# Optimization experiments

Measured on AMD Instinct MI355X. Metric: run time of the kernel, lower is better.

## Reference

```python
import jax, jax.numpy as jnp
import numpy as np

B = 131072
FEATURES = 64
NUM_BINS = 10
HIDDEN = 512
TAIL_BOUND = 1.0
MIN_BIN_WIDTH = 1e-3
MIN_BIN_HEIGHT = 1e-3
MIN_DERIVATIVE = 1e-3

# alternating mask [1,0,1,0,...]: mask>0 -> transform features, mask<=0 -> identity features
TRANSFORM_IDX = np.arange(0, FEATURES, 2)
IDENTITY_IDX = np.arange(1, FEATURES, 2)
D_ID = len(IDENTITY_IDX)   # 32
D_TR = len(TRANSFORM_IDX)  # 32
PARAM_PER_FEAT = 3 * NUM_BINS - 1  # tails='linear' -> 29
PARAM_DIM = D_TR * PARAM_PER_FEAT  # 928


def setup_inputs() -> dict:
    key = jax.random.key(0)
    k = jax.random.split(key, 3)
    x = jax.random.normal(k[0], (B, FEATURES), jnp.float32)
    W1 = jax.random.normal(k[1], (D_ID, HIDDEN), jnp.float32) / np.sqrt(D_ID)
    b1 = jnp.zeros((HIDDEN,), jnp.float32)
    W2 = jax.random.normal(k[2], (HIDDEN, PARAM_DIM), jnp.float32) / np.sqrt(HIDDEN)
    b2 = jnp.zeros((PARAM_DIM,), jnp.float32)
    return {"x": x, "W1": W1, "b1": b1, "W2": W2, "b2": b2}


def _rqs(x, uw, uh, ud):
    """Unconstrained rational-quadratic spline with linear tails, forward direction.
    x: [B, D]; uw, uh: [B, D, NUM_BINS]; ud: [B, D, NUM_BINS-1].
    Returns (outputs [B,D], logabsdet [B,D])."""
    inside = (x >= -TAIL_BOUND) & (x <= TAIL_BOUND)
    xc = jnp.clip(x, -TAIL_BOUND, TAIL_BOUND)
    # pad derivatives so boundary derivatives equal 1 (softplus(const)+md == 1)
    const = np.log(np.exp(1.0 - MIN_DERIVATIVE) - 1.0)
    ud = jnp.pad(ud, [(0, 0), (0, 0), (1, 1)], constant_values=const)
    nb = NUM_BINS

    widths = jax.nn.softmax(uw, axis=-1)
    widths = MIN_BIN_WIDTH + (1 - MIN_BIN_WIDTH * nb) * widths
    cumw = jnp.pad(jnp.cumsum(widths, axis=-1), [(0, 0), (0, 0), (1, 0)])
    cumw = 2 * TAIL_BOUND * cumw - TAIL_BOUND
    cumw = cumw.at[..., 0].set(-TAIL_BOUND).at[..., -1].set(TAIL_BOUND)
    widths = cumw[..., 1:] - cumw[..., :-1]

    derivs = MIN_DERIVATIVE + jax.nn.softplus(ud)  # [B, D, nb+1]

    heights = jax.nn.softmax(uh, axis=-1)
    heights = MIN_BIN_HEIGHT + (1 - MIN_BIN_HEIGHT * nb) * heights
    cumh = jnp.pad(jnp.cumsum(heights, axis=-1), [(0, 0), (0, 0), (1, 0)])
    cumh = 2 * TAIL_BOUND * cumh - TAIL_BOUND
    cumh = cumh.at[..., 0].set(-TAIL_BOUND).at[..., -1].set(TAIL_BOUND)
    heights = cumh[..., 1:] - cumh[..., :-1]

    # bin search (nflows-style searchsorted with eps on last edge)
    locs = cumw.at[..., -1].add(1e-6)
    idx = jnp.sum((xc[..., None] >= locs).astype(jnp.int32), axis=-1) - 1
    idx = jnp.clip(idx, 0, nb - 1)[..., None]

    g = lambda t: jnp.take_along_axis(t, idx, axis=-1)[..., 0]
    in_cw = g(cumw)
    in_w = g(widths)
    in_ch = g(cumh)
    in_h = g(heights)
    in_delta = g(heights / widths)
    d_k = g(derivs)
    d_k1 = jnp.take_along_axis(derivs, idx + 1, axis=-1)[..., 0]

    theta = (xc - in_cw) / in_w
    t1m = theta * (1 - theta)
    numer = in_h * (in_delta * theta ** 2 + d_k * t1m)
    denom = in_delta + (d_k + d_k1 - 2 * in_delta) * t1m
    y = in_ch + numer / denom
    dnum = in_delta ** 2 * (d_k1 * theta ** 2 + 2 * in_delta * t1m + d_k * (1 - theta) ** 2)
    lad = jnp.log(dnum) - 2 * jnp.log(denom)
    # linear tails: identity outside [-B, B], logabsdet 0
    return jnp.where(inside, y, x), jnp.where(inside, lad, 0.0)


def reference(x, W1, b1, W2, b2):
    ident = x[:, IDENTITY_IDX]   # [B, D_ID]
    trans = x[:, TRANSFORM_IDX]  # [B, D_TR]
    # transform_net: 1-hidden-layer MLP
    h = jax.nn.relu(ident @ W1 + b1)
    params = (h @ W2 + b2).reshape(x.shape[0], D_TR, PARAM_PER_FEAT)
    scale = 1.0 / np.sqrt(HIDDEN)  # hidden_features scaling branch
    uw = params[..., :NUM_BINS] * scale
    uh = params[..., NUM_BINS:2 * NUM_BINS] * scale
    ud = params[..., 2 * NUM_BINS:]
    y_tr, lad = _rqs(trans, uw, uh, ud)
    logabsdet = jnp.sum(lad, axis=1)  # sum_except_batch
    out = jnp.zeros_like(x).at[:, IDENTITY_IDX].set(ident).at[:, TRANSFORM_IDX].set(y_tr)
    ot_cost = jnp.sum((x - out) ** 2, axis=-1)
    return out, logabsdet, ot_cost
```

## Files before the change

### kernel.cpp

```cpp
#include <hip/hip_runtime.h>
#include <math.h>

#define NROWS 131072
#define BM 64
#define NBLK (NROWS / BM)
#define NB 10
#define PPF 29
#define NRAW 928
#define NPAD 1024
#define HID 512
#define THREADS 512

typedef _Float16 half8 __attribute__((ext_vector_type(8)));
typedef _Float16 half4v __attribute__((ext_vector_type(4)));
typedef float f32x4 __attribute__((ext_vector_type(4)));

#define W1T_OFF (NPAD * HID * 2)

#define LDS_B0 65536
#define LDS_B1 98304
#define LDS_TOTAL 131072
#define PSTR 937

__global__ __launch_bounds__(256) void prep_w2(const float* __restrict__ W2,
                                               _Float16* __restrict__ W2T) {
    __shared__ float tile[32][33];
    const int kt = blockIdx.x >> 5;
    const int nt = blockIdx.x & 31;
    const int t = threadIdx.x;
    const int j = t & 31;
    const int i0 = t >> 5;
    #pragma unroll
    for (int q = 0; q < 4; ++q) {
        int i = i0 + q * 8;
        int n = nt * 32 + j;
        float v = 0.f;
        if (n < NRAW) v = W2[(size_t)(kt * 32 + i) * NRAW + n];
        tile[i][j] = v;
    }
    __syncthreads();
    const int n_l = t >> 3;
    const int k_l = (t & 7) * 4;
    half4v o;
    o[0] = (_Float16)tile[k_l + 0][n_l];
    o[1] = (_Float16)tile[k_l + 1][n_l];
    o[2] = (_Float16)tile[k_l + 2][n_l];
    o[3] = (_Float16)tile[k_l + 3][n_l];
    *(half4v*)&W2T[(size_t)(nt * 32 + n_l) * HID + kt * 32 + k_l] = o;
}

__global__ __launch_bounds__(256) void prep_w1(const float* __restrict__ W1,
                                               _Float16* __restrict__ W1T) {
    int idx = blockIdx.x * 256 + threadIdx.x;
    int n = idx >> 5, k = idx & 31;
    W1T[n * 32 + k] = (_Float16)W1[k * HID + n];
}

__device__ __forceinline__ float softplusf(float v) {
    return fmaxf(v, 0.f) + log1pf(expf(-fabsf(v)));
}

__device__ __forceinline__ void rqs_one(const float* p, float xv, float& yo,
                                        float& lad_o, float& ot_o) {
    const float SCALE = 0.04419417382415922f;
    float uw[NB];
    #pragma unroll
    for (int j = 0; j < NB; ++j) uw[j] = p[j] * SCALE;
    float mw = uw[0];
    #pragma unroll
    for (int j = 1; j < NB; ++j) mw = fmaxf(mw, uw[j]);
    float sw = 0.f;
    #pragma unroll
    for (int j = 0; j < NB; ++j) { uw[j] = expf(uw[j] - mw); sw += uw[j]; }
    float invw = 1.f / sw;
    float cw[NB + 1];
    cw[0] = -1.f;
    float cum = 0.f;
    #pragma unroll
    for (int j = 0; j < NB; ++j) {
        cum += 0.001f + 0.99f * uw[j] * invw;
        cw[j + 1] = 2.f * cum - 1.f;
    }
    cw[NB] = 1.f;

    float uh[NB];
    #pragma unroll
    for (int j = 0; j < NB; ++j) uh[j] = p[NB + j] * SCALE;
    float mh = uh[0];
    #pragma unroll
    for (int j = 1; j < NB; ++j) mh = fmaxf(mh, uh[j]);
    float sh = 0.f;
    #pragma unroll
    for (int j = 0; j < NB; ++j) { uh[j] = expf(uh[j] - mh); sh += uh[j]; }
    float invh = 1.f / sh;
    float ch[NB + 1];
    ch[0] = -1.f;
    float cumh = 0.f;
    #pragma unroll
    for (int j = 0; j < NB; ++j) {
        cumh += 0.001f + 0.99f * uh[j] * invh;
        ch[j + 1] = 2.f * cumh - 1.f;
    }
    ch[NB] = 1.f;

    float dv[NB + 1];
    dv[0] = 1.0f;
    dv[NB] = 1.0f;
    #pragma unroll
    for (int j = 0; j < NB - 1; ++j) dv[j + 1] = 0.001f + softplusf(p[2 * NB + j]);

    float xc = fminf(fmaxf(xv, -1.f), 1.f);
    int idx = 0;
    #pragma unroll
    for (int j = 1; j <= NB - 1; ++j) idx += (xc >= cw[j]) ? 1 : 0;
    float in_cw = cw[0], cwn = cw[1];
    float in_ch = ch[0], chn = ch[1];
    float dk = dv[0], dk1 = dv[1];
    #pragma unroll
    for (int j = 1; j <= NB - 1; ++j) {
        bool cnd = (idx >= j);
        in_cw = cnd ? cw[j] : in_cw;
        cwn   = cnd ? cw[j + 1] : cwn;
        in_ch = cnd ? ch[j] : in_ch;
        chn   = cnd ? ch[j + 1] : chn;
        dk    = cnd ? dv[j] : dk;
        dk1   = cnd ? dv[j + 1] : dk1;
    }
    float in_w  = cwn - in_cw;
    float in_h  = chn - in_ch;
    float delta = in_h / in_w;
    float th    = (xc - in_cw) / in_w;
    float t1m   = th * (1.f - th);
    float th2   = th * th;
    float numer = in_h * (delta * th2 + dk * t1m);
    float denom = delta + (dk + dk1 - 2.f * delta) * t1m;
    float y     = in_ch + numer / denom;
    float omt   = 1.f - th;
    float dnum  = delta * delta * (dk1 * th2 + 2.f * delta * t1m + dk * omt * omt);
    float lad   = logf(dnum) - 2.f * logf(denom);

    bool inside = (xv >= -1.f) && (xv <= 1.f);
    yo = inside ? y : xv;
    lad_o = inside ? lad : 0.f;
    float dd = xv - yo;
    ot_o = dd * dd;
}

__global__ __launch_bounds__(THREADS, 2) void flow_main(
    const float* __restrict__ x,
    const float* __restrict__ b1,
    const float* __restrict__ b2,
    const _Float16* __restrict__ W2T,
    const _Float16* __restrict__ W1T,
    float* __restrict__ out,
    float* __restrict__ lad_out,
    float* __restrict__ ot_out)
{
    __shared__ __align__(16) char smem[LDS_TOTAL];
    __shared__ float sb2[NRAW];
    const int tid = threadIdx.x;
    const int w   = tid >> 6;
    const int l   = tid & 63;
    const int l15 = l & 15;
    const int g   = l >> 4;
    const int row0 = blockIdx.x * BM;

    {
        const float4* xv = (const float4*)(x + (size_t)row0 * 64);
        float4* ov = (float4*)(out + (size_t)row0 * 64);
        ov[tid] = xv[tid];
        ov[tid + 512] = xv[tid + 512];
    }
    sb2[tid] = b2[tid];
    if (tid < NRAW - 512) sb2[tid + 512] = b2[tid + 512];

    float4 st[4];
    #pragma unroll
    for (int q = 0; q < 4; ++q) {
        int s = tid + 512 * q;
        int nl = s >> 2, gg = s & 3;
        st[q] = *(const float4*)((const char*)W2T + (size_t)nl * (HID * 2) + gg * 16);
    }

    {
        const int mt1 = w >> 1;
        const int nbase = (w & 1) * 256;
        half8 a1;
        {
            const float4* xr = (const float4*)(x + (size_t)(row0 + mt1 * 16 + l15) * 64 + g * 16);
            float4 q0 = xr[0], q1 = xr[1], q2 = xr[2], q3 = xr[3];
            a1[0] = (_Float16)q0.y; a1[1] = (_Float16)q0.w;
            a1[2] = (_Float16)q1.y; a1[3] = (_Float16)q1.w;
            a1[4] = (_Float16)q2.y; a1[5] = (_Float16)q2.w;
            a1[6] = (_Float16)q3.y; a1[7] = (_Float16)q3.w;
        }
        #pragma unroll
        for (int j = 0; j < 16; ++j) {
            int n = nbase + j * 16 + l15;
            half8 bf = *(const half8*)((const char*)W1T + (size_t)n * 64 + g * 16);
            f32x4 c = {0.f, 0.f, 0.f, 0.f};
            c = __builtin_amdgcn_mfma_f32_16x16x32_f16(a1, bf, c, 0, 0, 0);
            float bias = b1[n];
            int srow_base = mt1 * 16 + g * 4;
            int sslot = n >> 3;
            #pragma unroll
            for (int r = 0; r < 4; ++r) {
                float hv = fmaxf(c[r] + bias, 0.f);
                int row = srow_base + r;
                int addr = row * 1024 + ((sslot ^ (row & 7)) << 4) + (n & 7) * 2;
                *(_Float16*)(smem + addr) = (_Float16)hv;
            }
        }
    }
    #pragma unroll
    for (int q = 0; q < 4; ++q) {
        int s = tid + 512 * q;
        int nl = s >> 2, gg = s & 3;
        int line = nl >> 1;
        int pos = (gg + 4 * (nl & 1)) ^ (line & 7);
        *(float4*)(smem + LDS_B0 + line * 128 + pos * 16) = st[q];
    }
    __syncthreads();

    f32x4 acc[4][8];
    #pragma unroll
    for (int mt = 0; mt < 4; ++mt)
        #pragma unroll
        for (int i = 0; i < 8; ++i) acc[mt][i] = (f32x4){0.f, 0.f, 0.f, 0.f};

    const int bn0 = w * 16 + l15;

    for (int ks = 0; ks < 16; ++ks) {
        #pragma unroll
        for (int q = 0; q < 4; ++q) {
            int s = tid + 512 * q;
            int nl = s >> 2, gg = s & 3;
            st[q] = *(const float4*)((const char*)W2T +
                     (size_t)(512 + nl) * (HID * 2) + ks * 64 + gg * 16);
        }
        half8 af[4];
        #pragma unroll
        for (int mt = 0; mt < 4; ++mt) {
            int row = mt * 16 + l15;
            int sslot = ks * 4 + g;
            af[mt] = *(const half8*)(smem + row * 1024 + ((sslot ^ (row & 7)) << 4));
        }
        #pragma unroll
        for (int i2 = 0; i2 < 4; ++i2) {
            int nloc = bn0 + i2 * 128;
            int line = nloc >> 1;
            int pos = (g + 4 * (nloc & 1)) ^ (line & 7);
            half8 bf = *(const half8*)(smem + LDS_B0 + line * 128 + pos * 16);
            acc[0][i2] = __builtin_amdgcn_mfma_f32_16x16x32_f16(af[0], bf, acc[0][i2], 0, 0, 0);
            acc[1][i2] = __builtin_amdgcn_mfma_f32_16x16x32_f16(af[1], bf, acc[1][i2], 0, 0, 0);
            acc[2][i2] = __builtin_amdgcn_mfma_f32_16x16x32_f16(af[2], bf, acc[2][i2], 0, 0, 0);
            acc[3][i2] = __builtin_amdgcn_mfma_f32_16x16x32_f16(af[3], bf, acc[3][i2], 0, 0, 0);
        }
        #pragma unroll
        for (int q = 0; q < 4; ++q) {
            int s = tid + 512 * q;
            int nl = s >> 2, gg = s & 3;
            int line = nl >> 1;
            int pos = (gg + 4 * (nl & 1)) ^ (line & 7);
            *(float4*)(smem + LDS_B1 + line * 128 + pos * 16) = st[q];
        }
        __syncthreads();

        if (ks < 15) {
            #pragma unroll
            for (int q = 0; q < 4; ++q) {
                int s = tid + 512 * q;
                int nl = s >> 2, gg = s & 3;
                st[q] = *(const float4*)((const char*)W2T +
                         (size_t)nl * (HID * 2) + (ks + 1) * 64 + gg * 16);
            }
        }
        #pragma unroll
        for (int i2 = 0; i2 < 4; ++i2) {
            int nloc = bn0 + i2 * 128;
            int line = nloc >> 1;
            int pos = (g + 4 * (nloc & 1)) ^ (line & 7);
            half8 bf = *(const half8*)(smem + LDS_B1 + line * 128 + pos * 16);
            acc[0][4 + i2] = __builtin_amdgcn_mfma_f32_16x16x32_f16(af[0], bf, acc[0][4 + i2], 0, 0, 0);
            acc[1][4 + i2] = __builtin_amdgcn_mfma_f32_16x16x32_f16(af[1], bf, acc[1][4 + i2], 0, 0, 0);
            acc[2][4 + i2] = __builtin_amdgcn_mfma_f32_16x16x32_f16(af[2], bf, acc[2][4 + i2], 0, 0, 0);
            acc[3][4 + i2] = __builtin_amdgcn_mfma_f32_16x16x32_f16(af[3], bf, acc[3][4 + i2], 0, 0, 0);
        }
        if (ks < 15) {
            #pragma unroll
            for (int q = 0; q < 4; ++q) {
                int s = tid + 512 * q;
                int nl = s >> 2, gg = s & 3;
                int line = nl >> 1;
                int pos = (gg + 4 * (nl & 1)) ^ (line & 7);
                *(float4*)(smem + LDS_B0 + line * 128 + pos * 16) = st[q];
            }
        }
        __syncthreads();
    }

    #pragma unroll
    for (int mh = 0; mh < 2; ++mh) {
        __syncthreads();
        #pragma unroll
        for (int mt2 = 0; mt2 < 2; ++mt2) {
            #pragma unroll
            for (int i = 0; i < 8; ++i) {
                int ntile = w + 8 * i;
                if (ntile < 58) {
                    int n = ntile * 16 + l15;
                    int prow = mt2 * 16 + g * 4;
                    #pragma unroll
                    for (int r = 0; r < 4; ++r) {
                        *(float*)(smem + ((prow + r) * PSTR + n) * 4) =
                            acc[mh * 2 + mt2][i][r];
                    }
                }
            }
        }
        __syncthreads();

        int row_l = tid >> 4;
        int grow = row0 + mh * 32 + row_l;
        float lads[2], ots[2];
        #pragma unroll
        for (int ff = 0; ff < 2; ++ff) {
            int f = (tid & 15) * 2 + ff;
            float p[PPF];
            #pragma unroll
            for (int j = 0; j < PPF; ++j)
                p[j] = *(const float*)(smem + (row_l * PSTR + f * PPF + j) * 4)
                       + sb2[f * PPF + j];
            float xv = x[(size_t)grow * 64 + 2 * f];
            float yo, lo, oo;
            rqs_one(p, xv, yo, lo, oo);
            out[(size_t)grow * 64 + 2 * f] = yo;
            lads[ff] = lo;
            ots[ff] = oo;
        }
        float ladp = lads[0] + lads[1];
        float otp  = ots[0] + ots[1];
        #pragma unroll
        for (int m = 1; m < 16; m <<= 1) {
            ladp += __shfl_xor(ladp, m);
            otp  += __shfl_xor(otp, m);
        }
        if ((tid & 15) == 0) {
            lad_out[grow] = ladp;
            ot_out[grow]  = otp;
        }
    }
}

extern "C" void kernel_launch(void* const* d_in, const int* in_sizes, int n_in,
                              void* d_out, int out_size, void* d_ws, size_t ws_size,
                              hipStream_t stream) {
    const float* x  = (const float*)d_in[0];
    const float* W1 = (const float*)d_in[1];
    const float* b1 = (const float*)d_in[2];
    const float* W2 = (const float*)d_in[3];
    const float* b2 = (const float*)d_in[4];
    float* out = (float*)d_out;
    float* lad = out + (size_t)NROWS * 64;
    float* otc = lad + NROWS;

    char* wsb = (char*)d_ws;
    _Float16* W2T = (_Float16*)wsb;
    _Float16* W1T = (_Float16*)(wsb + W1T_OFF);

    hipLaunchKernelGGL(prep_w2, dim3(512), dim3(256), 0, stream, W2, W2T);
    hipLaunchKernelGGL(prep_w1, dim3(64), dim3(256), 0, stream, W1, W1T);
    hipLaunchKernelGGL(flow_main, dim3(NBLK), dim3(THREADS), 0, stream,
                       x, b1, b2, W2T, W1T, out, lad, otc);
}
```

Measured before the change: 491.7 us.

## Hold A fragments in registers and stream W2 directly from global memory

The second GEMM no longer stages W2 tiles in LDS with double-buffering and barriers. Each wave keeps its 16-row slice of the hidden activations in registers across all K steps and reads W2 fragments straight from global memory (L2-resident) for half of the output columns. LDS shrinks to a padded hidden buffer that is reused for the parameter epilogue, which now runs in four 16-row passes with one row per 32 lanes. This removes LDS traffic and barriers from the main loop, but each wave now loads W2 from global/L2 instead of sharing it through LDS, raises register pressure with 32 accumulators plus 16 fragments, and splits columns unevenly between the two wave halves (16 vs 13 tile pairs).

```diff
diff --git a/kernel.cpp b/kernel.cpp
--- a/kernel.cpp
+++ b/kernel.cpp
@@ -17,10 +17,9 @@
 
 #define W1T_OFF (NPAD * HID * 2)
 
-#define LDS_B0 65536
-#define LDS_B1 98304
-#define LDS_TOTAL 131072
-#define PSTR 937
+#define HSTR 1040
+#define PSTR 936
+#define SMEM_BYTES (BM * HSTR)
 
 __global__ __launch_bounds__(256) void prep_w2(const float* __restrict__ W2,
                                                _Float16* __restrict__ W2T) {
@@ -146,6 +145,23 @@
     ot_o = dd * dd;
 }
 
+template<int NPAIR>
+__device__ __forceinline__ void gemm2_run(f32x4 (&acc)[32], const half8 (&afk)[16],
+                                          const char* w2b) {
+    #pragma unroll
+    for (int jp = 0; jp < NPAIR; ++jp) {
+        const char* p0 = w2b + (size_t)jp * 32768;
+        const char* p1 = p0 + 16384;
+        #pragma unroll
+        for (int ks = 0; ks < 16; ++ks) {
+            half8 bf0 = *(const half8*)(p0 + ks * 64);
+            half8 bf1 = *(const half8*)(p1 + ks * 64);
+            acc[2 * jp]     = __builtin_amdgcn_mfma_f32_16x16x32_f16(afk[ks], bf0, acc[2 * jp], 0, 0, 0);
+            acc[2 * jp + 1] = __builtin_amdgcn_mfma_f32_16x16x32_f16(afk[ks], bf1, acc[2 * jp + 1], 0, 0, 0);
+        }
+    }
+}
+
 __global__ __launch_bounds__(THREADS, 2) void flow_main(
     const float* __restrict__ x,
     const float* __restrict__ b1,
@@ -156,7 +172,7 @@
     float* __restrict__ lad_out,
     float* __restrict__ ot_out)
 {
-    __shared__ __align__(16) char smem[LDS_TOTAL];
+    __shared__ __align__(16) char smem[SMEM_BYTES];
     __shared__ float sb2[NRAW];
     const int tid = threadIdx.x;
     const int w   = tid >> 6;
@@ -164,6 +180,8 @@
     const int l15 = l & 15;
     const int g   = l >> 4;
     const int row0 = blockIdx.x * BM;
+    const int mt1 = w >> 1;
+    const int nh  = w & 1;
 
     {
         const float4* xv = (const float4*)(x + (size_t)row0 * 64);
@@ -174,17 +192,8 @@
     sb2[tid] = b2[tid];
     if (tid < NRAW - 512) sb2[tid + 512] = b2[tid + 512];
 
-    float4 st[4];
-    #pragma unroll
-    for (int q = 0; q < 4; ++q) {
-        int s = tid + 512 * q;
-        int nl = s >> 2, gg = s & 3;
-        st[q] = *(const float4*)((const char*)W2T + (size_t)nl * (HID * 2) + gg * 16);
-    }
-
     {
-        const int mt1 = w >> 1;
-        const int nbase = (w & 1) * 256;
+        const int nbase = nh * 256;
         half8 a1;
         {
             const float4* xr = (const float4*)(x + (size_t)(row0 + mt1 * 16 + l15) * 64 + g * 16);
@@ -201,151 +210,68 @@
             f32x4 c = {0.f, 0.f, 0.f, 0.f};
             c = __builtin_amdgcn_mfma_f32_16x16x32_f16(a1, bf, c, 0, 0, 0);
             float bias = b1[n];
-            int srow_base = mt1 * 16 + g * 4;
-            int sslot = n >> 3;
             #pragma unroll
             for (int r = 0; r < 4; ++r) {
                 float hv = fmaxf(c[r] + bias, 0.f);
-                int row = srow_base + r;
-                int addr = row * 1024 + ((sslot ^ (row & 7)) << 4) + (n & 7) * 2;
-                *(_Float16*)(smem + addr) = (_Float16)hv;
+                *(_Float16*)(smem + (mt1 * 16 + g * 4 + r) * HSTR + n * 2) = (_Float16)hv;
             }
         }
     }
+    __syncthreads();
+
+    half8 afk[16];
+    {
+        const char* abase = smem + (mt1 * 16 + l15) * HSTR + g * 16;
+        #pragma unroll
+        for (int ks = 0; ks < 16; ++ks)
+            afk[ks] = *(const half8*)(abase + ks * 64);
+    }
+
+    f32x4 acc[32];
+    #pragma unroll
+    for (int i = 0; i < 32; ++i) acc[i] = (f32x4){0.f, 0.f, 0.f, 0.f};
+
+    const char* w2b = (const char*)W2T + ((size_t)(nh * 512 + l15) * (HID * 2) + g * 16);
+    if (nh == 0) gemm2_run<16>(acc, afk, w2b);
+    else         gemm2_run<13>(acc, afk, w2b);
+
     #pragma unroll
     for (int q = 0; q < 4; ++q) {
-        int s = tid + 512 * q;
-        int nl = s >> 2, gg = s & 3;
-        int line = nl >> 1;
-        int pos = (gg + 4 * (nl & 1)) ^ (line & 7);
-        *(float4*)(smem + LDS_B0 + line * 128 + pos * 16) = st[q];
-    }
-    __syncthreads();
-
-    f32x4 acc[4][8];
-    #pragma unroll
-    for (int mt = 0; mt < 4; ++mt)
-        #pragma unroll
-        for (int i = 0; i < 8; ++i) acc[mt][i] = (f32x4){0.f, 0.f, 0.f, 0.f};
-
-    const int bn0 = w * 16 + l15;
-
-    for (int ks = 0; ks < 16; ++ks) {
-        #pragma unroll
-        for (int q = 0; q < 4; ++q) {
-            int s = tid + 512 * q;
-            int nl = s >> 2, gg = s & 3;
-            st[q] = *(const float4*)((const char*)W2T +
-                     (size_t)(512 + nl) * (HID * 2) + ks * 64 + gg * 16);
-        }
-        half8 af[4];
-        #pragma unroll
-        for (int mt = 0; mt < 4; ++mt) {
-            int row = mt * 16 + l15;
-            int sslot = ks * 4 + g;
-            af[mt] = *(const half8*)(smem + row * 1024 + ((sslot ^ (row & 7)) << 4));
-        }
-        #pragma unroll
-        for (int i2 = 0; i2 < 4; ++i2) {
-            int nloc = bn0 + i2 * 128;
-            int line = nloc >> 1;
-            int pos = (g + 4 * (nloc & 1)) ^ (line & 7);
-            half8 bf = *(const half8*)(smem + LDS_B0 + line * 128 + pos * 16);
-            acc[0][i2] = __builtin_amdgcn_mfma_f32_16x16x32_f16(af[0], bf, acc[0][i2], 0, 0, 0);
-            acc[1][i2] = __builtin_amdgcn_mfma_f32_16x16x32_f16(af[1], bf, acc[1][i2], 0, 0, 0);
-            acc[2][i2] = __builtin_amdgcn_mfma_f32_16x16x32_f16(af[2], bf, acc[2][i2], 0, 0, 0);
-            acc[3][i2] = __builtin_amdgcn_mfma_f32_16x16x32_f16(af[3], bf, acc[3][i2], 0, 0, 0);
-        }
-        #pragma unroll
-        for (int q = 0; q < 4; ++q) {
-            int s = tid + 512 * q;
-            int nl = s >> 2, gg = s & 3;
-            int line = nl >> 1;
-            int pos = (gg + 4 * (nl & 1)) ^ (line & 7);
-            *(float4*)(smem + LDS_B1 + line * 128 + pos * 16) = st[q];
-        }
         __syncthreads();
-
-        if (ks < 15) {
+        if (mt1 == q) {
             #pragma unroll
-            for (int q = 0; q < 4; ++q) {
-                int s = tid + 512 * q;
-                int nl = s >> 2, gg = s & 3;
-                st[q] = *(const float4*)((const char*)W2T +
-                         (size_t)nl * (HID * 2) + (ks + 1) * 64 + gg * 16);
-            }
-        }
-        #pragma unroll
-        for (int i2 = 0; i2 < 4; ++i2) {
-            int nloc = bn0 + i2 * 128;
-            int line = nloc >> 1;
-            int pos = (g + 4 * (nloc & 1)) ^ (line & 7);
-            half8 bf = *(const half8*)(smem + LDS_B1 + line * 128 + pos * 16);
-            acc[0][4 + i2] = __builtin_amdgcn_mfma_f32_16x16x32_f16(af[0], bf, acc[0][4 + i2], 0, 0, 0);
-            acc[1][4 + i2] = __builtin_amdgcn_mfma_f32_16x16x32_f16(af[1], bf, acc[1][4 + i2], 0, 0, 0);
-            acc[2][4 + i2] = __builtin_amdgcn_mfma_f32_16x16x32_f16(af[2], bf, acc[2][4 + i2], 0, 0, 0);
-            acc[3][4 + i2] = __builtin_amdgcn_mfma_f32_16x16x32_f16(af[3], bf, acc[3][4 + i2], 0, 0, 0);
-        }
-        if (ks < 15) {
-            #pragma unroll
-            for (int q = 0; q < 4; ++q) {
-                int s = tid + 512 * q;
-                int nl = s >> 2, gg = s & 3;
-                int line = nl >> 1;
-                int pos = (gg + 4 * (nl & 1)) ^ (line & 7);
-                *(float4*)(smem + LDS_B0 + line * 128 + pos * 16) = st[q];
-            }
-        }
-        __syncthreads();
-    }
-
-    #pragma unroll
-    for (int mh = 0; mh < 2; ++mh) {
-        __syncthreads();
-        #pragma unroll
-        for (int mt2 = 0; mt2 < 2; ++mt2) {
-            #pragma unroll
-            for (int i = 0; i < 8; ++i) {
-                int ntile = w + 8 * i;
-                if (ntile < 58) {
-                    int n = ntile * 16 + l15;
-                    int prow = mt2 * 16 + g * 4;
-                    #pragma unroll
-                    for (int r = 0; r < 4; ++r) {
-                        *(float*)(smem + ((prow + r) * PSTR + n) * 4) =
-                            acc[mh * 2 + mt2][i][r];
+            for (int j2 = 0; j2 < 32; ++j2) {
+                int n = nh * 512 + j2 * 16 + l15;
+                if (nh == 0 || j2 < 26) {
+                    if (n < NRAW) {
+                        #pragma unroll
+                        for (int r = 0; r < 4; ++r)
+                            *(float*)(smem + ((g * 4 + r) * PSTR + n) * 4) = acc[j2][r];
                     }
                 }
             }
         }
         __syncthreads();
 
-        int row_l = tid >> 4;
-        int grow = row0 + mh * 32 + row_l;
-        float lads[2], ots[2];
-        #pragma unroll
-        for (int ff = 0; ff < 2; ++ff) {
-            int f = (tid & 15) * 2 + ff;
-            float p[PPF];
-            #pragma unroll
-            for (int j = 0; j < PPF; ++j)
-                p[j] = *(const float*)(smem + (row_l * PSTR + f * PPF + j) * 4)
-                       + sb2[f * PPF + j];
-            float xv = x[(size_t)grow * 64 + 2 * f];
-            float yo, lo, oo;
-            rqs_one(p, xv, yo, lo, oo);
-            out[(size_t)grow * 64 + 2 * f] = yo;
-            lads[ff] = lo;
-            ots[ff] = oo;
-        }
-        float ladp = lads[0] + lads[1];
-        float otp  = ots[0] + ots[1];
-        #pragma unroll
-        for (int m = 1; m < 16; m <<= 1) {
+        int row_l = tid >> 5;
+        int f = tid & 31;
+        int grow = row0 + q * 16 + row_l;
+        float p[PPF];
+        #pragma unroll
+        for (int jj = 0; jj < PPF; ++jj)
+            p[jj] = *(const float*)(smem + (row_l * PSTR + f * PPF + jj) * 4)
+                    + sb2[f * PPF + jj];
+        float xv = x[(size_t)grow * 64 + 2 * f];
+        float yo, lo, oo;
+        rqs_one(p, xv, yo, lo, oo);
+        out[(size_t)grow * 64 + 2 * f] = yo;
+        float ladp = lo, otp = oo;
+        #pragma unroll
+        for (int m = 1; m < 32; m <<= 1) {
             ladp += __shfl_xor(ladp, m);
             otp  += __shfl_xor(otp, m);
         }
-        if ((tid & 15) == 0) {
+        if ((tid & 31) == 0) {
             lad_out[grow] = ladp;
             ot_out[grow]  = otp;
         }
```

Measured after the change: 1.207 ms. 146% more time.
